# Kernel tuning notes

Hardware: AMD Instinct MI355X
Metric: run time of the kernel (lower is better)

The kernel has to match this reference:

```python
import jax, jax.numpy as jnp
import numpy as np

EPS = 1e-6
ROPE_THETA = 10000.0
NUM_HEADS = 32
NUM_KV_HEADS = 8
HEAD_DIM = 128
HIDDEN = 4096
B, S = 2, 2048


def setup_inputs() -> dict:
    key = jax.random.key(0)
    ks = jax.random.split(key, 6)
    scale = 0.02
    return {
        "hidden_states": jax.random.normal(ks[0], (B, S, HIDDEN), dtype=jnp.float32),
        "position_ids": jnp.arange(S, dtype=jnp.int64 if jax.config.jax_enable_x64 else jnp.int32)[None, :],
        "Wq": jax.random.normal(ks[1], (HIDDEN, NUM_HEADS * HEAD_DIM), dtype=jnp.float32) * scale,
        "Wk": jax.random.normal(ks[2], (HIDDEN, NUM_KV_HEADS * HEAD_DIM), dtype=jnp.float32) * scale,
        "Wv": jax.random.normal(ks[3], (HIDDEN, NUM_KV_HEADS * HEAD_DIM), dtype=jnp.float32) * scale,
        "Wo": jax.random.normal(ks[4], (NUM_HEADS * HEAD_DIM, HIDDEN), dtype=jnp.float32) * scale,
        "q_norm_w": jnp.ones((HEAD_DIM,), dtype=jnp.float32),
        "k_norm_w": jnp.ones((HEAD_DIM,), dtype=jnp.float32),
    }


def _rms_norm(x, w):
    # RMSNorm over last dim (head_dim)
    var = jnp.mean(jnp.square(x), axis=-1, keepdims=True)
    return x * jax.lax.rsqrt(var + EPS) * w


def _rope(x, position_ids):
    # x: [B, H, S, D]; Llama-style half-split rotation
    d = x.shape[-1]
    inv_freq = 1.0 / (ROPE_THETA ** (jnp.arange(0, d, 2, dtype=jnp.float32) / d))  # [D/2]
    ang = position_ids[:, :, None].astype(jnp.float32) * inv_freq[None, None, :]   # [B, S, D/2]
    emb = jnp.concatenate([ang, ang], axis=-1)                                     # [B, S, D]
    cos = jnp.cos(emb)[:, None, :, :]
    sin = jnp.sin(emb)[:, None, :, :]
    x1, x2 = x[..., : d // 2], x[..., d // 2:]
    rot = jnp.concatenate([-x2, x1], axis=-1)
    return x * cos + rot * sin


def reference(hidden_states, position_ids, Wq, Wk, Wv, Wo, q_norm_w, k_norm_w):
    b, s, _ = hidden_states.shape
    q = (hidden_states @ Wq).reshape(b, s, NUM_HEADS, HEAD_DIM).transpose(0, 2, 1, 3)
    k = (hidden_states @ Wk).reshape(b, s, NUM_KV_HEADS, HEAD_DIM).transpose(0, 2, 1, 3)
    v = (hidden_states @ Wv).reshape(b, s, NUM_KV_HEADS, HEAD_DIM).transpose(0, 2, 1, 3)

    q = _rms_norm(q, q_norm_w)
    k = _rms_norm(k, k_norm_w)

    q = _rope(q, position_ids)
    k = _rope(k, position_ids)

    groups = NUM_HEADS // NUM_KV_HEADS
    k = jnp.repeat(k, groups, axis=1)  # repeat_interleave along head dim
    v = jnp.repeat(v, groups, axis=1)

    scale = 1.0 / jnp.sqrt(jnp.float32(HEAD_DIM))
    scores = jnp.einsum("bhqd,bhkd->bhqk", q, k) * scale
    causal = jnp.tril(jnp.ones((s, s), dtype=bool))
    scores = jnp.where(causal[None, None], scores, jnp.finfo(scores.dtype).min)
    attn = jax.nn.softmax(scores, axis=-1)
    out = jnp.einsum("bhqk,bhkd->bhqd", attn, v)
    out = out.transpose(0, 2, 1, 3).reshape(b, s, NUM_HEADS * HEAD_DIM)
    return out @ Wo
```

## Files before the change

kernel.cpp:

```cpp
#include <hip/hip_runtime.h>
#include <stdint.h>
#include <stddef.h>

#define S_LEN 2048
#define BATCH 2
#define NHEADS 32
#define NKV 8
#define HD 128
#define HIDDEN 4096
#define T_TOK (BATCH * S_LEN)

typedef unsigned short u16;
typedef __attribute__((ext_vector_type(4))) float f32x4;
typedef __attribute__((ext_vector_type(16))) float f32x16;
typedef __attribute__((ext_vector_type(8))) short s16x8;
typedef __attribute__((ext_vector_type(4))) unsigned short u16x4;
typedef __attribute__((ext_vector_type(4))) unsigned int u32x4;

__device__ __forceinline__ u16 f2bf(float f) {
  unsigned int u = __builtin_bit_cast(unsigned int, f);
  unsigned int r = (u + 0x7FFFu + ((u >> 16) & 1u)) >> 16;
  return (u16)r;
}
__device__ __forceinline__ float bf2f(u16 h) {
  return __builtin_bit_cast(float, ((unsigned int)h) << 16);
}

__device__ __forceinline__ void gload16(const void* g, void* l) {
  __builtin_amdgcn_global_load_lds((__attribute__((address_space(1))) void*)g,
                                   (__attribute__((address_space(3))) void*)l,
                                   16, 0, 0);
}

__device__ __forceinline__ unsigned cvtpk(float a, float b) {
  unsigned r;
  asm("v_cvt_pk_bf16_f32 %0, %1, %2" : "=v"(r) : "v"(a), "v"(b));
  return r;
}
__device__ __forceinline__ void lohi_dup(unsigned W, unsigned& lo, unsigned& hi) {
  unsigned a = W, b = W;
  asm volatile("v_permlane32_swap_b32 %0, %1" : "+v"(a), "+v"(b));
  lo = a; hi = b;
}

__global__ __launch_bounds__(256) void k_convert(const float* __restrict__ in,
                                                 u16* __restrict__ out, int n8) {
  int i = blockIdx.x * 256 + threadIdx.x;
  if (i >= n8) return;
  float4 a = ((const float4*)in)[i * 2];
  float4 b = ((const float4*)in)[i * 2 + 1];
  u16x4 lo = {f2bf(a.x), f2bf(a.y), f2bf(a.z), f2bf(a.w)};
  u16x4 hi = {f2bf(b.x), f2bf(b.y), f2bf(b.z), f2bf(b.w)};
  ((u16x4*)out)[i * 2] = lo;
  ((u16x4*)out)[i * 2 + 1] = hi;
}

__global__ __launch_bounds__(256) void k_transpose_w(const float* __restrict__ W,
                                                     u16* __restrict__ Wt, int K,
                                                     int N, int outRowOff,
                                                     int outStride) {
  __shared__ float tl[32][33];
  int k0 = blockIdx.x * 32, n0 = blockIdx.y * 32;
  int t = threadIdx.x;
  int r = t >> 3, c4 = (t & 7) * 4;
  float4 v = *(const float4*)&W[(size_t)(k0 + r) * N + n0 + c4];
  tl[r][c4] = v.x; tl[r][c4 + 1] = v.y; tl[r][c4 + 2] = v.z; tl[r][c4 + 3] = v.w;
  __syncthreads();
  u16x4 o = {f2bf(tl[c4][r]), f2bf(tl[c4 + 1][r]), f2bf(tl[c4 + 2][r]),
             f2bf(tl[c4 + 3][r])};
  *(u16x4*)&Wt[(size_t)(outRowOff + n0 + r) * outStride + k0 + c4] = o;
}

__global__ __launch_bounds__(256) void k_rope_tab(const int* __restrict__ pos,
                                                  float* __restrict__ tab) {
  int i = blockIdx.x * 256 + threadIdx.x;
  int s = i >> 6, l = i & 63;
  float p = (float)pos[s];
  float ang = p * expf(-(float)l * 0.14391156516342163f);
  tab[s * 128 + l] = cosf(ang);
  tab[s * 128 + 64 + l] = sinf(ang);
}

template <typename OutT>
__global__ __launch_bounds__(512, 2) void k_gemm256(const u16* __restrict__ A,
                                                    const u16* __restrict__ Bt,
                                                    OutT* __restrict__ C,
                                                    int M, int N, int K) {
  __shared__ u16 As[2][16384];
  __shared__ u16 Bs[2][16384];
  int nbn = N >> 8;
  int nwg = gridDim.x;
  int orig = blockIdx.x;
  int q8 = nwg >> 3, r8 = nwg & 7;
  int xcd = orig & 7, sub = orig >> 3;
  int wgid = (xcd < r8 ? xcd * (q8 + 1) : r8 * (q8 + 1) + (xcd - r8) * q8) + sub;
  int bm = wgid / nbn, bn = wgid % nbn;
  int tid = threadIdx.x, wid = tid >> 6, lane = tid & 63;
  int wm = wid >> 2, wn = wid & 3;
  int g = lane >> 4, c = lane & 15;
  int l3 = lane >> 3, l7 = lane & 7;
  int xpos = (l7 ^ l3) * 8;

  f32x4 acc[8][4];
#pragma unroll
  for (int m = 0; m < 8; m++)
#pragma unroll
    for (int n = 0; n < 4; n++) acc[m][n] = (f32x4){0.f, 0.f, 0.f, 0.f};

  const u16* aSrc = A + (size_t)(bm * 256 + wid * 32 + l3) * K + xpos;
  const u16* bSrc = Bt + (size_t)(bn * 256 + wid * 32 + l3) * K + xpos;

#pragma unroll
  for (int j = 0; j < 4; j++) {
    gload16(aSrc + (size_t)(j * 8) * K, &As[0][(wid * 4 + j) * 512]);
    gload16(bSrc + (size_t)(j * 8) * K, &Bs[0][(wid * 4 + j) * 512]);
  }
  asm volatile("s_waitcnt vmcnt(0)" ::: "memory");
  __builtin_amdgcn_s_barrier();

  int nt = K >> 6;
  int swz = (c & 7);
  for (int t = 0; t < nt; t++) {
    int cur = t & 1;
    const u16* Ab = &As[cur][0];
    const u16* Bb = &Bs[cur][0];
    bool pre = (t + 1 < nt);
    size_t koff = (size_t)(t + 1) << 6;
#pragma unroll
    for (int p = 0; p < 4; p++) {
      const int mh = p & 1, ks = p >> 1;
      int sz = ((ks * 4 + g) ^ swz) * 8;
      s16x8 af[4], bf[4];
#pragma unroll
      for (int mi = 0; mi < 4; mi++)
        af[mi] = *(const s16x8*)&Ab[(wm * 128 + (mh * 4 + mi) * 16 + c) * 64 + sz];
#pragma unroll
      for (int n = 0; n < 4; n++)
        bf[n] = *(const s16x8*)&Bb[(wn * 64 + n * 16 + c) * 64 + sz];
      if (p < 2 && pre) {
#pragma unroll
        for (int j2 = 0; j2 < 2; j2++) {
          int j = p * 2 + j2;
          gload16(aSrc + (size_t)(j * 8) * K + koff, &As[cur ^ 1][(wid * 4 + j) * 512]);
          gload16(bSrc + (size_t)(j * 8) * K + koff, &Bs[cur ^ 1][(wid * 4 + j) * 512]);
        }
      }
      __builtin_amdgcn_s_barrier();
      asm volatile("s_waitcnt lgkmcnt(0)" ::: "memory");
      __builtin_amdgcn_sched_barrier(0);
      __builtin_amdgcn_s_setprio(1);
#pragma unroll
      for (int mi = 0; mi < 4; mi++)
#pragma unroll
        for (int n = 0; n < 4; n++)
          acc[mh * 4 + mi][n] = __builtin_amdgcn_mfma_f32_16x16x32_bf16(
              af[mi], bf[n], acc[mh * 4 + mi][n], 0, 0, 0);
      __builtin_amdgcn_s_setprio(0);
      if (p == 3 && pre)
        asm volatile("s_waitcnt vmcnt(0)" ::: "memory");
      __builtin_amdgcn_s_barrier();
    }
  }
#pragma unroll
  for (int m = 0; m < 8; m++)
#pragma unroll
    for (int n = 0; n < 4; n++) {
      size_t row = (size_t)bm * 256 + wm * 128 + m * 16 + g * 4;
      size_t col = (size_t)bn * 256 + wn * 64 + n * 16 + c;
#pragma unroll
      for (int r = 0; r < 4; r++) {
        float v = acc[m][n][r];
        if constexpr (sizeof(OutT) == 2)
          C[(row + r) * N + col] = (OutT)f2bf(v);
        else
          C[(row + r) * N + col] = (OutT)v;
      }
    }
}

__global__ __launch_bounds__(256) void k_rmsrope(u16* __restrict__ QK,
                                                 const float* __restrict__ w,
                                                 const float* __restrict__ tab,
                                                 int H, int rowStride) {
  int row = blockIdx.x * 4 + (threadIdx.x >> 6);
  int lane = threadIdx.x & 63;
  int t = row / H, h = row - t * H;
  int s = t & (S_LEN - 1);
  u16* p = QK + (size_t)t * rowStride + h * HD;
  float x1 = bf2f(p[lane]), x2 = bf2f(p[lane + 64]);
  float ss = x1 * x1 + x2 * x2;
#pragma unroll
  for (int o = 32; o >= 1; o >>= 1) ss += __shfl_xor(ss, o);
  float inv = rsqrtf(ss * (1.0f / 128.0f) + 1e-6f);
  float y1 = x1 * inv * w[lane], y2 = x2 * inv * w[lane + 64];
  float cs = tab[s * 128 + lane], sn = tab[s * 128 + 64 + lane];
  p[lane] = f2bf(y1 * cs - y2 * sn);
  p[lane + 64] = f2bf(y2 * cs + y1 * sn);
}

__global__ __launch_bounds__(256) void k_transpose_v(const u16* __restrict__ KV,
                                                     u16* __restrict__ Vt) {
  __shared__ u16 tl[32][40];
  int bkh = blockIdx.x;
  int s0 = blockIdx.y * 32, d0 = blockIdx.z * 32;
  int b = bkh >> 3, kh = bkh & 7;
  int t = threadIdx.x, r = t >> 3, c4 = (t & 7) * 4;
  const u16* src =
      KV + (size_t)(b * S_LEN + s0 + r) * 2048 + 1024 + kh * HD + d0 + c4;
  u16x4 v = *(const u16x4*)src;
  tl[r][c4] = v[0]; tl[r][c4 + 1] = v[1]; tl[r][c4 + 2] = v[2]; tl[r][c4 + 3] = v[3];
  __syncthreads();
  u16x4 o = {tl[c4][r], tl[c4 + 1][r], tl[c4 + 2][r], tl[c4 + 3][r]};
  *(u16x4*)&Vt[(size_t)(bkh * HD + d0 + r) * S_LEN + s0 + c4] = o;
}

__global__ __launch_bounds__(256) void k_attn(const u16* __restrict__ Q,
                                              const u16* __restrict__ KV,
                                              const u16* __restrict__ Vt,
                                              u16* __restrict__ Oact) {
  __shared__ u16 Ks[2][64 * 128];
  __shared__ u16 Vs[2][128 * 64];
  int bid = blockIdx.x;
  int qt = 15 - (bid >> 6);
  int bh = bid & 63;
  int h = bh & 31, b = bh >> 5;
  int kh = h >> 2;
  int w = threadIdx.x >> 6, lane = threadIdx.x & 63;
  int q31 = lane & 31, hh = lane >> 5;
  int qw0 = qt * 128 + w * 32;
  const float scale = 0.08838834764831845f;

  s16x8 qf[8];
  const u16* Qp = Q + (size_t)(b * S_LEN + qw0 + q31) * 4096 + h * HD + hh * 8;
#pragma unroll
  for (int dc = 0; dc < 8; dc++) {
    s16x8 raw = *(const s16x8*)(Qp + dc * 16);
#pragma unroll
    for (int e = 0; e < 8; e++)
      qf[dc][e] = (short)f2bf(bf2f((u16)raw[e]) * scale);
  }

  f32x16 o[4];
#pragma unroll
  for (int d = 0; d < 4; d++)
#pragma unroll
    for (int r = 0; r < 16; r++) o[d][r] = 0.f;
  float m = -3.0e38f, l = 0.f;

  const char* Kg = (const char*)(KV + (size_t)b * S_LEN * 2048 + kh * HD);
  const char* Vg = (const char*)(Vt + (size_t)(b * 8 + kh) * HD * S_LEN);

  int nch = 2 * qt + 2;

  {
    char* KsB = (char*)Ks[0];
    char* VsB = (char*)Vs[0];
#pragma unroll
    for (int j = 0; j < 4; j++) {
      int ins = w * 4 + j;
      int row = ins * 4 + (lane >> 4);
      int bc = ((lane & 15) * 16) ^ ((row & 7) << 4);
      gload16(Kg + (size_t)row * 4096 + bc, KsB + ins * 1024);
    }
#pragma unroll
    for (int j = 0; j < 4; j++) {
      int ins = w * 4 + j;
      int row = ins * 8 + (lane >> 3);
      int bc = ((lane & 7) * 16) ^ ((row & 7) << 4);
      gload16(Vg + (size_t)row * 4096 + bc, VsB + ins * 1024);
    }
  }

  int cur = 0;
  for (int ch = 0; ch < nch; ch++) {
    int kb = ch * 64;
    __syncthreads();
    if (ch + 1 < nch) {
      char* KsB = (char*)Ks[cur ^ 1];
      char* VsB = (char*)Vs[cur ^ 1];
      int kb2 = kb + 64;
#pragma unroll
      for (int j = 0; j < 4; j++) {
        int ins = w * 4 + j;
        int row = ins * 4 + (lane >> 4);
        int bc = ((lane & 15) * 16) ^ ((row & 7) << 4);
        gload16(Kg + (size_t)(kb2 + row) * 4096 + bc, KsB + ins * 1024);
      }
#pragma unroll
      for (int j = 0; j < 4; j++) {
        int ins = w * 4 + j;
        int row = ins * 8 + (lane >> 3);
        int bc = ((lane & 7) * 16) ^ ((row & 7) << 4);
        gload16(Vg + (size_t)row * 4096 + (size_t)kb2 * 2 + bc, VsB + ins * 1024);
      }
    }
    if (kb <= qw0 + 31) {
      char* KsB = (char*)Ks[cur];
      char* VsB = (char*)Vs[cur];
      f32x16 sA, sB;
#pragma unroll
      for (int r = 0; r < 16; r++) { sA[r] = 0.f; sB[r] = 0.f; }
      int sw = (q31 & 7) << 4;
      __builtin_amdgcn_s_setprio(1);
#pragma unroll
      for (int dc = 0; dc < 8; dc++) {
        s16x8 kfA = *(const s16x8*)(KsB + q31 * 256 + ((dc * 32 + hh * 16) ^ sw));
        s16x8 kfB = *(const s16x8*)(KsB + (32 + q31) * 256 + ((dc * 32 + hh * 16) ^ sw));
        sA = __builtin_amdgcn_mfma_f32_32x32x16_bf16(kfA, qf[dc], sA, 0, 0, 0);
        sB = __builtin_amdgcn_mfma_f32_32x32x16_bf16(kfB, qf[dc], sB, 0, 0, 0);
      }
      __builtin_amdgcn_s_setprio(0);
      if (kb + 63 > qw0) {
        int qa = qw0 + q31;
#pragma unroll
        for (int r = 0; r < 16; r++) {
          int krow = (r & 3) + 8 * (r >> 2) + 4 * hh;
          if (kb + krow > qa) sA[r] = -1e30f;
          if (kb + 32 + krow > qa) sB[r] = -1e30f;
        }
      }
      float mx = -3.0e38f;
#pragma unroll
      for (int r = 0; r < 16; r++) mx = fmaxf(mx, fmaxf(sA[r], sB[r]));
      mx = fmaxf(mx, __shfl_xor(mx, 32));
      if (!__all(mx - m <= 8.0f)) {
        float mnew = fmaxf(m, mx);
        float corr = __expf(m - mnew);
        l *= corr;
#pragma unroll
        for (int d = 0; d < 4; d++)
#pragma unroll
          for (int r = 0; r < 16; r++) o[d][r] *= corr;
        m = mnew;
      }
      float rs = 0.f;
#pragma unroll
      for (int r = 0; r < 16; r++) {
        sA[r] = __expf(sA[r] - m); rs += sA[r];
        sB[r] = __expf(sB[r] - m); rs += sB[r];
      }
      rs += __shfl_xor(rs, 32);
      l += rs;
#pragma unroll
      for (int st = 0; st < 2; st++) {
        unsigned Aw[8], Bw[8];
#pragma unroll
        for (int j = 0; j < 8; j++) {
          float p0 = st ? sB[2 * j] : sA[2 * j];
          float p1 = st ? sB[2 * j + 1] : sA[2 * j + 1];
          lohi_dup(cvtpk(p0, p1), Aw[j], Bw[j]);
        }
#pragma unroll
        for (int kc2 = 0; kc2 < 2; kc2++) {
          u32x4 wv;
          wv.x = hh ? Aw[kc2 * 4 + 2] : Aw[kc2 * 4 + 0];
          wv.y = hh ? Aw[kc2 * 4 + 3] : Aw[kc2 * 4 + 1];
          wv.z = hh ? Bw[kc2 * 4 + 2] : Bw[kc2 * 4 + 0];
          wv.w = hh ? Bw[kc2 * 4 + 3] : Bw[kc2 * 4 + 1];
          s16x8 pf = __builtin_bit_cast(s16x8, wv);
          int kc = st * 2 + kc2;
          __builtin_amdgcn_s_setprio(1);
#pragma unroll
          for (int d = 0; d < 4; d++) {
            int row = d * 32 + q31;
            int vsw = (row & 7) << 4;
            s16x8 vf = *(const s16x8*)(VsB + row * 128 + ((kc * 32 + hh * 16) ^ vsw));
            o[d] = __builtin_amdgcn_mfma_f32_32x32x16_bf16(vf, pf, o[d], 0, 0, 0);
          }
          __builtin_amdgcn_s_setprio(0);
        }
      }
    }
    cur ^= 1;
  }
  float linv = 1.0f / l;
  u16* Op = Oact + (size_t)(b * S_LEN + qw0 + q31) * 4096 + h * HD;
#pragma unroll
  for (int d = 0; d < 4; d++)
#pragma unroll
    for (int g4 = 0; g4 < 4; g4++) {
      int d0 = d * 32 + 8 * g4 + 4 * hh;
      u16x4 w4 = {f2bf(o[d][4 * g4 + 0] * linv), f2bf(o[d][4 * g4 + 1] * linv),
                  f2bf(o[d][4 * g4 + 2] * linv), f2bf(o[d][4 * g4 + 3] * linv)};
      *(u16x4*)(Op + d0) = w4;
    }
}

extern "C" void kernel_launch(void* const* d_in, const int* in_sizes, int n_in,
                              void* d_out, int out_size, void* d_ws,
                              size_t ws_size, hipStream_t stream) {
  (void)in_sizes; (void)n_in; (void)out_size; (void)ws_size;
  const float* X = (const float*)d_in[0];
  const int* pos = (const int*)d_in[1];
  const float* Wq = (const float*)d_in[2];
  const float* Wk = (const float*)d_in[3];
  const float* Wv = (const float*)d_in[4];
  const float* Wo = (const float*)d_in[5];
  const float* qw = (const float*)d_in[6];
  const float* kw = (const float*)d_in[7];
  float* out = (float*)d_out;
  char* ws = (char*)d_ws;

  const size_t MB = 1024ull * 1024ull;
  u16* Xb    = (u16*)(ws + 0 * MB);
  u16* WqT   = (u16*)(ws + 32 * MB);
  u16* WkvT  = (u16*)(ws + 64 * MB);
  u16* WoT   = (u16*)(ws + 80 * MB);
  u16* Qb    = (u16*)(ws + 112 * MB);
  u16* KVb   = (u16*)(ws + 144 * MB);
  u16* Vt    = (u16*)(ws + 160 * MB);
  u16* Oact  = (u16*)(ws + 168 * MB);
  float* tab = (float*)(ws + 200 * MB);

  k_convert<<<8192, 256, 0, stream>>>(X, Xb, (T_TOK * HIDDEN) / 8);
  k_transpose_w<<<dim3(128, 128), 256, 0, stream>>>(Wq, WqT, 4096, 4096, 0, 4096);
  k_transpose_w<<<dim3(128, 32), 256, 0, stream>>>(Wk, WkvT, 4096, 1024, 0, 4096);
  k_transpose_w<<<dim3(128, 32), 256, 0, stream>>>(Wv, WkvT, 4096, 1024, 1024, 4096);
  k_transpose_w<<<dim3(128, 128), 256, 0, stream>>>(Wo, WoT, 4096, 4096, 0, 4096);
  k_rope_tab<<<512, 256, 0, stream>>>(pos, tab);

  k_gemm256<u16><<<16 * 16, 512, 0, stream>>>(Xb, WqT, Qb, 4096, 4096, 4096);
  k_gemm256<u16><<<16 * 8, 512, 0, stream>>>(Xb, WkvT, KVb, 4096, 2048, 4096);

  k_rmsrope<<<(T_TOK * NHEADS) / 4, 256, 0, stream>>>(Qb, qw, tab, NHEADS, 4096);
  k_rmsrope<<<(T_TOK * NKV) / 4, 256, 0, stream>>>(KVb, kw, tab, NKV, 2048);

  k_transpose_v<<<dim3(16, 64, 4), 256, 0, stream>>>(KVb, Vt);

  k_attn<<<BATCH * NHEADS * (S_LEN / 128), 256, 0, stream>>>(Qb, KVb, Vt, Oact);

  k_gemm256<float><<<16 * 16, 512, 0, stream>>>(Oact, WoT, out, 4096, 4096, 4096);
}
```

Baseline: 699.9 us.

## Restructure GEMM main loop into quadrant-phased schedule with deeper B prefetch

Reworks the 256x256 bf16 GEMM inner loop into four quadrant phases (A-upper/lower × B-left/right). Global loads are interleaved per phase, with A prefetched one tile ahead and B prefetched two tiles ahead into the current buffer. Tiles are loaded in half-tile chunks, and partial vmcnt waits replace full drains. The goal is to hide global-load latency and cut LDS reads by reusing A/B fragments across MFMA phases, at the cost of a more fragile barrier and waitcnt protocol.

```diff
diff --git a/kernel.cpp b/kernel.cpp
--- a/kernel.cpp
+++ b/kernel.cpp
@@ -85,7 +85,7 @@
 __global__ __launch_bounds__(512, 2) void k_gemm256(const u16* __restrict__ A,
                                                     const u16* __restrict__ Bt,
                                                     OutT* __restrict__ C,
-                                                    int M, int N, int K) {
+                                                    int N, int K) {
   __shared__ u16 As[2][16384];
   __shared__ u16 Bs[2][16384];
   int nbn = N >> 8;
@@ -99,7 +99,8 @@
   int wm = wid >> 2, wn = wid & 3;
   int g = lane >> 4, c = lane & 15;
   int l3 = lane >> 3, l7 = lane & 7;
-  int xpos = (l7 ^ l3) * 8;
+  int swz = c & 7;
+  int xunit = (l7 ^ l3) * 8;
 
   f32x4 acc[8][4];
 #pragma unroll
@@ -107,60 +108,128 @@
 #pragma unroll
     for (int n = 0; n < 4; n++) acc[m][n] = (f32x4){0.f, 0.f, 0.f, 0.f};
 
-  const u16* aSrc = A + (size_t)(bm * 256 + wid * 32 + l3) * K + xpos;
-  const u16* bSrc = Bt + (size_t)(bn * 256 + wid * 32 + l3) * K + xpos;
-
-#pragma unroll
-  for (int j = 0; j < 4; j++) {
-    gload16(aSrc + (size_t)(j * 8) * K, &As[0][(wid * 4 + j) * 512]);
-    gload16(bSrc + (size_t)(j * 8) * K, &Bs[0][(wid * 4 + j) * 512]);
+  const u16* aBase = A + (size_t)(bm * 256 + wid * 16 + l3) * K + xunit;
+  const u16* bBase = Bt + (size_t)(bn * 256 + wid * 16 + l3) * K + xunit;
+
+  auto stgA = [&](int buf, int h, int j, size_t koff) {
+    gload16(aBase + (size_t)(h * 128 + j * 8) * K + koff,
+            &As[buf][(h * 128 + wid * 16 + j * 8) * 64]);
+  };
+  auto stgB = [&](int buf, int h, int j, size_t koff) {
+    gload16(bBase + (size_t)(h * 128 + j * 8) * K + koff,
+            &Bs[buf][(h * 128 + wid * 16 + j * 8) * 64]);
+  };
+
+  int nt = K >> 6;
+#pragma unroll
+  for (int j = 0; j < 2; j++) {
+    stgA(0, 0, j, 0); stgA(0, 1, j, 0);
+    stgB(0, 0, j, 0); stgB(0, 1, j, 0);
   }
-  asm volatile("s_waitcnt vmcnt(0)" ::: "memory");
+#pragma unroll
+  for (int j = 0; j < 2; j++) { stgB(1, 0, j, 64); stgB(1, 1, j, 64); }
+  asm volatile("s_waitcnt vmcnt(4)" ::: "memory");
   __builtin_amdgcn_s_barrier();
 
-  int nt = K >> 6;
-  int swz = (c & 7);
   for (int t = 0; t < nt; t++) {
-    int cur = t & 1;
-    const u16* Ab = &As[cur][0];
-    const u16* Bb = &Bs[cur][0];
-    bool pre = (t + 1 < nt);
-    size_t koff = (size_t)(t + 1) << 6;
-#pragma unroll
-    for (int p = 0; p < 4; p++) {
-      const int mh = p & 1, ks = p >> 1;
-      int sz = ((ks * 4 + g) ^ swz) * 8;
-      s16x8 af[4], bf[4];
-#pragma unroll
-      for (int mi = 0; mi < 4; mi++)
-        af[mi] = *(const s16x8*)&Ab[(wm * 128 + (mh * 4 + mi) * 16 + c) * 64 + sz];
-#pragma unroll
-      for (int n = 0; n < 4; n++)
-        bf[n] = *(const s16x8*)&Bb[(wn * 64 + n * 16 + c) * 64 + sz];
-      if (p < 2 && pre) {
-#pragma unroll
-        for (int j2 = 0; j2 < 2; j2++) {
-          int j = p * 2 + j2;
-          gload16(aSrc + (size_t)(j * 8) * K + koff, &As[cur ^ 1][(wid * 4 + j) * 512]);
-          gload16(bSrc + (size_t)(j * 8) * K + koff, &Bs[cur ^ 1][(wid * 4 + j) * 512]);
-        }
-      }
-      __builtin_amdgcn_s_barrier();
-      asm volatile("s_waitcnt lgkmcnt(0)" ::: "memory");
-      __builtin_amdgcn_sched_barrier(0);
-      __builtin_amdgcn_s_setprio(1);
-#pragma unroll
-      for (int mi = 0; mi < 4; mi++)
-#pragma unroll
-        for (int n = 0; n < 4; n++)
-          acc[mh * 4 + mi][n] = __builtin_amdgcn_mfma_f32_16x16x32_bf16(
-              af[mi], bf[n], acc[mh * 4 + mi][n], 0, 0, 0);
-      __builtin_amdgcn_s_setprio(0);
-      if (p == 3 && pre)
-        asm volatile("s_waitcnt vmcnt(0)" ::: "memory");
-      __builtin_amdgcn_s_barrier();
-    }
+    int cb = t & 1;
+    const u16* Ab = &As[cb][0];
+    const u16* Bb = &Bs[cb][0];
+    size_t k1 = (size_t)(t + 1) << 6;
+    size_t k2 = (size_t)(t + 2) << 6;
+    bool s1 = (t + 1 < nt), s2 = (t + 2 < nt);
+    s16x8 af[8], bf0[4], bf1[4];
+
+#pragma unroll
+    for (int mi = 0; mi < 4; mi++)
+#pragma unroll
+      for (int ks = 0; ks < 2; ks++)
+        af[mi * 2 + ks] = *(const s16x8*)&Ab[(wm * 128 + mi * 16 + c) * 64 +
+                                             (((ks * 4 + g) ^ swz) * 8)];
+#pragma unroll
+    for (int nj = 0; nj < 2; nj++)
+#pragma unroll
+      for (int ks = 0; ks < 2; ks++)
+        bf0[nj * 2 + ks] = *(const s16x8*)&Bb[(wn * 64 + nj * 16 + c) * 64 +
+                                              (((ks * 4 + g) ^ swz) * 8)];
+    if (s1) { stgA(cb ^ 1, 0, 0, k1); stgA(cb ^ 1, 0, 1, k1); }
+    __builtin_amdgcn_s_barrier();
+    asm volatile("s_waitcnt lgkmcnt(0)" ::: "memory");
+    __builtin_amdgcn_sched_barrier(0);
+    __builtin_amdgcn_s_setprio(1);
+#pragma unroll
+    for (int mi = 0; mi < 4; mi++)
+#pragma unroll
+      for (int nj = 0; nj < 2; nj++)
+#pragma unroll
+        for (int ks = 0; ks < 2; ks++)
+          acc[mi][nj] = __builtin_amdgcn_mfma_f32_16x16x32_bf16(
+              af[mi * 2 + ks], bf0[nj * 2 + ks], acc[mi][nj], 0, 0, 0);
+    __builtin_amdgcn_s_setprio(0);
+    __builtin_amdgcn_s_barrier();
+
+#pragma unroll
+    for (int nj = 0; nj < 2; nj++)
+#pragma unroll
+      for (int ks = 0; ks < 2; ks++)
+        bf1[nj * 2 + ks] = *(const s16x8*)&Bb[(wn * 64 + (2 + nj) * 16 + c) * 64 +
+                                              (((ks * 4 + g) ^ swz) * 8)];
+    if (s1) { stgA(cb ^ 1, 1, 0, k1); stgA(cb ^ 1, 1, 1, k1); }
+    __builtin_amdgcn_s_barrier();
+    asm volatile("s_waitcnt lgkmcnt(0)" ::: "memory");
+    __builtin_amdgcn_sched_barrier(0);
+    __builtin_amdgcn_s_setprio(1);
+#pragma unroll
+    for (int mi = 0; mi < 4; mi++)
+#pragma unroll
+      for (int nj = 0; nj < 2; nj++)
+#pragma unroll
+        for (int ks = 0; ks < 2; ks++)
+          acc[mi][2 + nj] = __builtin_amdgcn_mfma_f32_16x16x32_bf16(
+              af[mi * 2 + ks], bf1[nj * 2 + ks], acc[mi][2 + nj], 0, 0, 0);
+    __builtin_amdgcn_s_setprio(0);
+    __builtin_amdgcn_s_barrier();
+
+#pragma unroll
+    for (int mi = 0; mi < 4; mi++)
+#pragma unroll
+      for (int ks = 0; ks < 2; ks++)
+        af[mi * 2 + ks] = *(const s16x8*)&Ab[(wm * 128 + 64 + mi * 16 + c) * 64 +
+                                             (((ks * 4 + g) ^ swz) * 8)];
+    if (s2) { stgB(cb, 0, 0, k2); stgB(cb, 0, 1, k2); }
+    __builtin_amdgcn_s_barrier();
+    asm volatile("s_waitcnt lgkmcnt(0)" ::: "memory");
+    __builtin_amdgcn_sched_barrier(0);
+    __builtin_amdgcn_s_setprio(1);
+#pragma unroll
+    for (int mi = 0; mi < 4; mi++)
+#pragma unroll
+      for (int nj = 0; nj < 2; nj++)
+#pragma unroll
+        for (int ks = 0; ks < 2; ks++)
+          acc[4 + mi][nj] = __builtin_amdgcn_mfma_f32_16x16x32_bf16(
+              af[mi * 2 + ks], bf0[nj * 2 + ks], acc[4 + mi][nj], 0, 0, 0);
+    __builtin_amdgcn_s_setprio(0);
+    __builtin_amdgcn_s_barrier();
+
+    if (s2) { stgB(cb, 1, 0, k2); stgB(cb, 1, 1, k2); }
+    __builtin_amdgcn_s_setprio(1);
+#pragma unroll
+    for (int mi = 0; mi < 4; mi++)
+#pragma unroll
+      for (int nj = 0; nj < 2; nj++)
+#pragma unroll
+        for (int ks = 0; ks < 2; ks++)
+          acc[4 + mi][2 + nj] = __builtin_amdgcn_mfma_f32_16x16x32_bf16(
+              af[mi * 2 + ks], bf1[nj * 2 + ks], acc[4 + mi][2 + nj], 0, 0, 0);
+    __builtin_amdgcn_s_setprio(0);
+    if (s2)
+      asm volatile("s_waitcnt vmcnt(4)" ::: "memory");
+    else if (s1)
+      asm volatile("s_waitcnt vmcnt(0)" ::: "memory");
+    __builtin_amdgcn_s_barrier();
   }
+
 #pragma unroll
   for (int m = 0; m < 8; m++)
 #pragma unroll
@@ -419,8 +488,8 @@
   k_transpose_w<<<dim3(128, 128), 256, 0, stream>>>(Wo, WoT, 4096, 4096, 0, 4096);
   k_rope_tab<<<512, 256, 0, stream>>>(pos, tab);
 
-  k_gemm256<u16><<<16 * 16, 512, 0, stream>>>(Xb, WqT, Qb, 4096, 4096, 4096);
-  k_gemm256<u16><<<16 * 8, 512, 0, stream>>>(Xb, WkvT, KVb, 4096, 2048, 4096);
+  k_gemm256<u16><<<16 * 16, 512, 0, stream>>>(Xb, WqT, Qb, 4096, 4096);
+  k_gemm256<u16><<<16 * 8, 512, 0, stream>>>(Xb, WkvT, KVb, 2048, 4096);
 
   k_rmsrope<<<(T_TOK * NHEADS) / 4, 256, 0, stream>>>(Qb, qw, tab, NHEADS, 4096);
   k_rmsrope<<<(T_TOK * NKV) / 4, 256, 0, stream>>>(KVb, kw, tab, NKV, 2048);
@@ -429,5 +498,5 @@
 
   k_attn<<<BATCH * NHEADS * (S_LEN / 128), 256, 0, stream>>>(Qb, KVb, Vt, Oact);
 
-  k_gemm256<float><<<16 * 16, 512, 0, stream>>>(Oact, WoT, out, 4096, 4096, 4096);
-}
+  k_gemm256<float><<<16 * 16, 512, 0, stream>>>(Oact, WoT, out, 4096, 4096);
+}
```

Result: faster. 653.2 us (-6.7%).
